# Optimization experiments

Measured on AMD Instinct MI355X. Metric: run time of the kernel, lower is better.

The kernel has to match this reference:

```python
import jax, jax.numpy as jnp
import numpy as np

F_IN = 128
H = 512


def _uniform(key, shape, stdv):
    return jax.random.uniform(key, shape, jnp.float32, -stdv, stdv)


def setup_inputs() -> dict:
    key = jax.random.key(0)
    ks = jax.random.split(key, 20)
    B, T, F = 512, 96, F_IN
    x = jax.random.normal(ks[0], (B, T, F), jnp.float32)
    mask = jax.random.randint(ks[1], (B, T, F), 0, 2).astype(jnp.int32)
    sH = 1.0 / np.sqrt(H)
    sF = 1.0 / np.sqrt(F)
    inp = {
        'x': x,
        'mask': mask,
        # TemporalDecay h: W [H, F], b [H]
        'Wdh': _uniform(ks[2], (H, F), sH), 'bdh': _uniform(ks[3], (H,), sH),
        # TemporalDecay x (diag): W [F, F], b [F]
        'Wdx': _uniform(ks[4], (F, F), sF), 'bdx': _uniform(ks[5], (F,), sF),
        # hist_reg Linear(H, F)
        'Wh': _uniform(ks[6], (F, H), sH), 'bh': _uniform(ks[7], (F,), sH),
        # feat_reg: W [F, F] (off-diagonal mask), b [F]
        'Wf': _uniform(ks[8], (F, F), sF), 'bf': _uniform(ks[9], (F,), sF),
        # weight_combine Linear(2F, F)
        'Wc': _uniform(ks[10], (F, 2 * F), 1.0 / np.sqrt(2 * F)),
        'bc': _uniform(ks[11], (F,), 1.0 / np.sqrt(2 * F)),
        # LSTMCell(2F, H): torch gate order i, f, g, o
        'Wih': _uniform(ks[12], (4 * H, 2 * F), sH),
        'Whh': _uniform(ks[13], (4 * H, H), sH),
        'bih': _uniform(ks[14], (4 * H,), sH),
        'bhh': _uniform(ks[15], (4 * H,), sH),
    }
    return inp


def _rits_forward(x, m, Wdh, bdh, Wdx, bdx, Wh, bh, Wf, bf, Wc, bc, Wih, Whh, bih, bhh):
    B, T, F = x.shape
    eye = jnp.eye(F, dtype=x.dtype)
    Wf_m = Wf * (1.0 - eye)
    Wdx_m = Wdx * eye         # diagonal TemporalDecay

    # compute_delta (freq=1): delta[0]=0; delta[i]=m[i-1]+ (1-m[i-1])*(delta[i-1]+1)
    m_tm = jnp.swapaxes(m, 0, 1)  # [T, B, F]
    def dstep(prev, mp):
        nxt = mp + (1.0 - mp) * (prev + 1.0)
        return nxt, nxt
    _, drest = jax.lax.scan(dstep, jnp.zeros((B, F), x.dtype), m_tm[:-1])
    delta_tm = jnp.concatenate([jnp.zeros((1, B, F), x.dtype), drest], axis=0)

    x_tm = jnp.swapaxes(x, 0, 1)  # [T, B, F]

    def step(carry, inp):
        h, c = carry
        x_s, m_s, d = inp
        gamma_h = jnp.exp(-jax.nn.relu(d @ Wdh.T + bdh))          # [B, H]
        x_h = h @ Wh.T + bh                                        # [B, F]
        x_c = m_s * x_s + (1.0 - m_s) * x_h
        h = h * gamma_h
        z_h = x_c @ Wf_m.T + bf
        gamma_x = jnp.exp(-jax.nn.relu(d @ Wdx_m.T + bdx))
        alpha = jax.nn.sigmoid(jnp.concatenate([gamma_x, m_s], axis=1) @ Wc.T + bc)
        c_h = alpha * z_h + (1.0 - alpha) * x_h
        c_c = m_s * x_s + (1.0 - m_s) * c_h
        inputs = jnp.concatenate([c_c, m_s], axis=1)               # [B, 2F]
        gates = inputs @ Wih.T + bih + h @ Whh.T + bhh             # [B, 4H]
        i_g, f_g, g_g, o_g = jnp.split(gates, 4, axis=1)
        c = jax.nn.sigmoid(f_g) * c + jax.nn.sigmoid(i_g) * jnp.tanh(g_g)
        h = jax.nn.sigmoid(o_g) * jnp.tanh(c)
        return (h, c), (c_c, c_h, z_h, x_h)

    h0 = jnp.zeros((B, H), x.dtype)
    c0 = jnp.zeros((B, H), x.dtype)
    _, (c_c, c_h, z_h, x_h) = jax.lax.scan(step, (h0, c0), (x_tm, m_tm, delta_tm))
    # back to [B, T, F]
    tr = lambda a: jnp.swapaxes(a, 0, 1)
    return tr(c_c), tr(c_h), tr(z_h), tr(x_h)


def reference(x, mask, Wdh, bdh, Wdx, bdx, Wh, bh, Wf, bf, Wc, bc, Wih, Whh, bih, bhh):
    m = mask.astype(x.dtype)
    imputation, c_h, z_h, x_h = _rits_forward(
        x, m, Wdh, bdh, Wdx, bdx, Wh, bh, Wf, bf, Wc, bc, Wih, Whh, bih, bhh)
    return (imputation, (c_h, z_h, x_h))
```

## Files before the change

kernel.cpp:

```cpp
#include <hip/hip_runtime.h>
#include <cstdint>
#include <cstddef>

#define BB 512
#define TT 96
#define FF 128
#define HH 512
#define BTF 6291456
#define BH  262144

typedef unsigned short ushort_t;
typedef __attribute__((ext_vector_type(8))) short bf16x8;
typedef __attribute__((ext_vector_type(4))) float f32x4;

static constexpr size_t OFF_FLAGS = 0;
static constexpr size_t OFF_WDXD  = 2048;
static constexpr size_t OFF_DELTA = 4096;
static constexpr size_t OFF_MBF   = OFF_DELTA + 12582912;
static constexpr size_t OFF_ALPHA = OFF_MBF   + 12582912;
static constexpr size_t OFF_GH    = OFF_ALPHA + 12582912;
static constexpr size_t OFF_H     = OFF_GH    + 50331648;
static constexpr size_t OFF_HDEC  = OFF_H     + 2097152;
static constexpr size_t OFF_CCBF  = OFF_HDEC  + 1048576;

__device__ __forceinline__ float bf2f(ushort_t u) {
  union { unsigned u; float f; } c; c.u = ((unsigned)u) << 16; return c.f;
}
__device__ __forceinline__ ushort_t f2bf(float f) {
  union { float f; unsigned u; } c; c.f = f;
  unsigned x = c.u;
  unsigned r = (x + 0x7FFFu + ((x >> 16) & 1u)) >> 16;
  return (ushort_t)r;
}
__device__ __forceinline__ float lo2f(unsigned p) {
  union { unsigned u; float f; } c; c.u = p << 16; return c.f;
}
__device__ __forceinline__ float hi2f(unsigned p) {
  union { unsigned u; float f; } c; c.u = p & 0xffff0000u; return c.f;
}
__device__ __forceinline__ float sigm(float v) { return 1.0f / (1.0f + __expf(-v)); }

__device__ __forceinline__ bf16x8 cload16(const ushort_t* p) {
  union { unsigned long long q[2]; bf16x8 v; } u;
  unsigned long long* a = (unsigned long long*)p;
  u.q[0] = __hip_atomic_load(a,     __ATOMIC_RELAXED, __HIP_MEMORY_SCOPE_AGENT);
  u.q[1] = __hip_atomic_load(a + 1, __ATOMIC_RELAXED, __HIP_MEMORY_SCOPE_AGENT);
  return u.v;
}
__device__ __forceinline__ float cloadf(const float* p) {
  unsigned v = __hip_atomic_load((const unsigned*)p, __ATOMIC_RELAXED, __HIP_MEMORY_SCOPE_AGENT);
  union { unsigned u; float f; } c; c.u = v; return c.f;
}
__device__ __forceinline__ void cstore8(void* p, unsigned long long v) {
  __hip_atomic_store((unsigned long long*)p, v, __ATOMIC_RELAXED, __HIP_MEMORY_SCOPE_AGENT);
}
__device__ __forceinline__ void cstore4(void* p, unsigned v) {
  __hip_atomic_store((unsigned*)p, v, __ATOMIC_RELAXED, __HIP_MEMORY_SCOPE_AGENT);
}
__device__ __forceinline__ void cstore2(ushort_t* p, ushort_t v) {
  __hip_atomic_store(p, v, __ATOMIC_RELAXED, __HIP_MEMORY_SCOPE_AGENT);
}
__device__ __forceinline__ float rdlane_f(float v, int sl) {
  return __int_as_float(__builtin_amdgcn_readlane(__float_as_int(v), sl));
}

__global__ void k_cvt(const float* __restrict__ Wdx, char* __restrict__ ws) {
  int tid = threadIdx.x;
  unsigned* fl = (unsigned*)(ws + OFF_FLAGS);
  fl[tid] = 0; fl[256 + tid] = 0;
  float* wdxd = (float*)(ws + OFF_WDXD);
  if (tid < FF) wdxd[tid] = Wdx[tid * (FF + 1)];
}

__global__ void k_prep(const int* __restrict__ mask, char* __restrict__ ws) {
  ushort_t* delta = (ushort_t*)(ws + OFF_DELTA);
  ushort_t* mbf   = (ushort_t*)(ws + OFF_MBF);
  int gtid = blockIdx.x * 256 + threadIdx.x;
  int b = gtid >> 7, f = gtid & 127;
  const int* mrow = mask + (size_t)b * (TT * FF) + f;
  float dprev = 0.0f;
  for (int t = 0; t < TT; ++t) {
    float d;
    if (t == 0) d = 0.0f;
    else {
      int mp = mrow[(t - 1) * FF];
      d = mp ? 1.0f : dprev + 1.0f;
    }
    dprev = d;
    delta[((size_t)t * BB + b) * FF + f] = f2bf(d);
    int mc = mrow[t * FF];
    mbf[(size_t)b * (TT * FF) + t * FF + f] = f2bf((float)mc);
  }
}

__global__ __launch_bounds__(256, 4) void k_gh(const float* __restrict__ Wdh,
                                               const float* __restrict__ bdh,
                                               char* __restrict__ ws) {
  __shared__ ushort_t A_lds[64 * 136];
  __shared__ ushort_t B_lds[64 * 136];
  const ushort_t* delta = (const ushort_t*)(ws + OFF_DELTA);
  ushort_t* gh = (ushort_t*)(ws + OFF_GH);
  int tid = threadIdx.x;
  int m0 = blockIdx.x * 64;
  int n0 = blockIdx.y * 64;
  for (int v = tid; v < 1024; v += 256) {
    int row = v >> 4, seg = v & 15;
    *(uint4*)&A_lds[row * 136 + seg * 8] =
        *(const uint4*)(delta + ((size_t)(m0 + row)) * FF + seg * 8);
  }
  for (int v = tid; v < 1024; v += 256) {
    int n = v >> 4, seg = v & 15;
    const float* src = Wdh + (size_t)(n0 + n) * FF + seg * 8;
    ushort_t tmp[8];
#pragma unroll
    for (int j = 0; j < 8; ++j) tmp[j] = f2bf(src[j]);
    *(uint4*)&B_lds[n * 136 + seg * 8] = *(const uint4*)tmp;
  }
  __syncthreads();
  int wave = tid >> 6, lane = tid & 63, quad = lane >> 4, lan = lane & 15;
  int mt = wave;
  f32x4 acc[4];
#pragma unroll
  for (int nt = 0; nt < 4; ++nt) acc[nt] = (f32x4){0.f, 0.f, 0.f, 0.f};
  const ushort_t* ab = &A_lds[(mt * 16 + lan) * 136 + quad * 8];
#pragma unroll
  for (int kk = 0; kk < 4; ++kk) {
    bf16x8 af = *(const bf16x8*)(ab + kk * 32);
#pragma unroll
    for (int nt = 0; nt < 4; ++nt) {
      bf16x8 bfv = *(const bf16x8*)(&B_lds[(nt * 16 + lan) * 136 + kk * 32 + quad * 8]);
      acc[nt] = __builtin_amdgcn_mfma_f32_16x16x32_bf16(af, bfv, acc[nt], 0, 0, 0);
    }
  }
#pragma unroll
  for (int nt = 0; nt < 4; ++nt) {
#pragma unroll
    for (int r = 0; r < 4; ++r) {
      int mg = m0 + mt * 16 + quad * 4 + r;
      int nc = n0 + nt * 16 + lan;
      float v = acc[nt][r] + bdh[nc];
      gh[(size_t)mg * HH + nc] = f2bf(__expf(-fmaxf(v, 0.0f)));
    }
  }
}

__global__ __launch_bounds__(256, 4) void k_al(const float* __restrict__ Wc,
                                               const float* __restrict__ bc,
                                               const float* __restrict__ bdx,
                                               char* __restrict__ ws) {
  __shared__ ushort_t A_lds[64 * 136];
  __shared__ ushort_t B_lds[64 * 136];
  const ushort_t* delta = (const ushort_t*)(ws + OFF_DELTA);
  const ushort_t* mbf   = (const ushort_t*)(ws + OFF_MBF);
  const float* wdxd     = (const float*)(ws + OFF_WDXD);
  ushort_t* alpha = (ushort_t*)(ws + OFF_ALPHA);
  int tid = threadIdx.x;
  int m0 = blockIdx.x * 64;
  int n0 = blockIdx.y * 64;
  int wave = tid >> 6, lane = tid & 63, quad = lane >> 4, lan = lane & 15;
  int mt = wave;
  f32x4 acc[4];
#pragma unroll
  for (int nt = 0; nt < 4; ++nt) acc[nt] = (f32x4){0.f, 0.f, 0.f, 0.f};
  for (int c = 0; c < 2; ++c) {
    __syncthreads();
    if (c == 0) {
      for (int v = tid; v < 1024; v += 256) {
        int row = v >> 4, seg = v & 15;
        int mg = m0 + row;
        ushort_t tmp[8];
#pragma unroll
        for (int j = 0; j < 8; ++j) {
          int k = seg * 8 + j;
          float d = bf2f(delta[(size_t)mg * FF + k]);
          float g = __expf(-fmaxf(fmaf(d, wdxd[k], bdx[k]), 0.0f));
          tmp[j] = f2bf(g);
        }
        *(uint4*)&A_lds[row * 136 + seg * 8] = *(const uint4*)tmp;
      }
    } else {
      for (int v = tid; v < 1024; v += 256) {
        int row = v >> 4, seg = v & 15;
        int mg = m0 + row;
        int t = mg >> 9, b = mg & 511;
        *(uint4*)&A_lds[row * 136 + seg * 8] =
            *(const uint4*)(mbf + ((size_t)b * TT + t) * FF + seg * 8);
      }
    }
    for (int v = tid; v < 1024; v += 256) {
      int n = v >> 4, seg = v & 15;
      const float* src = Wc + (size_t)(n0 + n) * 256 + c * 128 + seg * 8;
      ushort_t tmp[8];
#pragma unroll
      for (int j = 0; j < 8; ++j) tmp[j] = f2bf(src[j]);
      *(uint4*)&B_lds[n * 136 + seg * 8] = *(const uint4*)tmp;
    }
    __syncthreads();
    const ushort_t* ab = &A_lds[(mt * 16 + lan) * 136 + quad * 8];
#pragma unroll
    for (int kk = 0; kk < 4; ++kk) {
      bf16x8 af = *(const bf16x8*)(ab + kk * 32);
#pragma unroll
      for (int nt = 0; nt < 4; ++nt) {
        bf16x8 bfv = *(const bf16x8*)(&B_lds[(nt * 16 + lan) * 136 + kk * 32 + quad * 8]);
        acc[nt] = __builtin_amdgcn_mfma_f32_16x16x32_bf16(af, bfv, acc[nt], 0, 0, 0);
      }
    }
  }
#pragma unroll
  for (int nt = 0; nt < 4; ++nt) {
#pragma unroll
    for (int r = 0; r < 4; ++r) {
      int mg = m0 + mt * 16 + quad * 4 + r;
      int nc = n0 + nt * 16 + lan;
      float v = acc[nt][r] + bc[nc];
      alpha[(size_t)mg * FF + nc] = f2bf(sigm(v));
    }
  }
}

__device__ __forceinline__ void bar_arrive(unsigned* cnt) {
  __syncthreads();
  if (threadIdx.x == 0)
    __hip_atomic_fetch_add(cnt, 1u, __ATOMIC_RELAXED, __HIP_MEMORY_SCOPE_AGENT);
}
__device__ __forceinline__ void bar_wait(unsigned* cnt, unsigned target) {
  if (threadIdx.x == 0) {
    while (__hip_atomic_load(cnt, __ATOMIC_RELAXED, __HIP_MEMORY_SCOPE_AGENT) < target)
      __builtin_amdgcn_s_sleep(1);
  }
  __syncthreads();
}

__global__ __launch_bounds__(512, 2) void k_main(
    const float* __restrict__ x, const int* __restrict__ mask,
    const float* __restrict__ Wh, const float* __restrict__ Wf,
    const float* __restrict__ bh, const float* __restrict__ bfr,
    const float* __restrict__ Wih, const float* __restrict__ Whh,
    const float* __restrict__ bih, const float* __restrict__ bhh,
    float* __restrict__ out, char* __restrict__ ws) {
  extern __shared__ char smem[];
  ushort_t* W_lds    = (ushort_t*)smem;
  float* gates_lds   = (float*)(smem + 99328);
  float* bias_lds    = (float*)(smem + 134144);
  float* xh_part     = (float*)(smem + 134400);
  float* xc_s        = (float*)(smem + 142592);

  unsigned* cnts = (unsigned*)(ws + OFF_FLAGS);
  const ushort_t* alpha = (const ushort_t*)(ws + OFF_ALPHA);
  const ushort_t* gh    = (const ushort_t*)(ws + OFF_GH);
  const ushort_t* mbf   = (const ushort_t*)(ws + OFF_MBF);
  float*    hws  = (float*)(ws + OFF_H);
  ushort_t* hdws = (ushort_t*)(ws + OFF_HDEC);
  ushort_t* ccbf = (ushort_t*)(ws + OFF_CCBF);

  const int tid  = threadIdx.x;
  const int wg   = blockIdx.x;
  const int g    = wg & 7;
  const int mwg  = wg >> 3;
  const int ng   = mwg;
  const int wave = tid >> 6, lane = tid & 63, quad = lane >> 4, lan = lane & 15;
  const int mt = wave & 3, khalf = wave >> 2;
  const int r0 = g * 64 + mwg * 2;
  const int arow = g * 64 + mt * 16 + lan;

  unsigned* cntA = cnts + (g * 2 + 0) * 32;
  unsigned* cntB = cnts + (g * 2 + 1) * 32;

  for (int q = tid; q < 4096; q += 512) {
    int n = q >> 6, kq = (q & 63) * 4;
    int r = (n >> 4) * 512 + ng * 16 + (n & 15);
    float4 v = *(const float4*)(Wih + (size_t)r * 256 + kq);
    ushort_t t4[4] = { f2bf(v.x), f2bf(v.y), f2bf(v.z), f2bf(v.w) };
    *(uint2*)&W_lds[n * 776 + kq] = *(const uint2*)t4;
  }
  for (int q = tid; q < 8192; q += 512) {
    int n = q >> 7, kq = (q & 127) * 4;
    int r = (n >> 4) * 512 + ng * 16 + (n & 15);
    float4 v = *(const float4*)(Whh + (size_t)r * 512 + kq);
    ushort_t t4[4] = { f2bf(v.x), f2bf(v.y), f2bf(v.z), f2bf(v.w) };
    *(uint2*)&W_lds[n * 776 + 256 + kq] = *(const uint2*)t4;
  }
  if (tid < 64) {
    int r = (tid >> 4) * 512 + ng * 16 + (tid & 15);
    bias_lds[tid] = bih[r] + bhh[r];
  }

  unsigned wh_p[64];
  {
    const float* s0 = Wh + (size_t)lane * HH + 64 * wave;
    const float* s1 = Wh + (size_t)(lane + 64) * HH + 64 * wave;
#pragma unroll
    for (int i4 = 0; i4 < 16; ++i4) {
      float4 a = *(const float4*)(s0 + i4 * 4);
      float4 b = *(const float4*)(s1 + i4 * 4);
      wh_p[i4 * 4 + 0] = ((unsigned)f2bf(a.x)) | (((unsigned)f2bf(b.x)) << 16);
      wh_p[i4 * 4 + 1] = ((unsigned)f2bf(a.y)) | (((unsigned)f2bf(b.y)) << 16);
      wh_p[i4 * 4 + 2] = ((unsigned)f2bf(a.z)) | (((unsigned)f2bf(b.z)) << 16);
      wh_p[i4 * 4 + 3] = ((unsigned)f2bf(a.w)) | (((unsigned)f2bf(b.w)) << 16);
    }
  }
  unsigned wf_p[16];
  {
    const float* s0 = Wf + (size_t)lane * FF + 16 * wave;
    const float* s1 = Wf + (size_t)(lane + 64) * FF + 16 * wave;
#pragma unroll
    for (int i4 = 0; i4 < 4; ++i4) {
      float4 a = *(const float4*)(s0 + i4 * 4);
      float4 b = *(const float4*)(s1 + i4 * 4);
      wf_p[i4 * 4 + 0] = ((unsigned)f2bf(a.x)) | (((unsigned)f2bf(b.x)) << 16);
      wf_p[i4 * 4 + 1] = ((unsigned)f2bf(a.y)) | (((unsigned)f2bf(b.y)) << 16);
      wf_p[i4 * 4 + 2] = ((unsigned)f2bf(a.z)) | (((unsigned)f2bf(b.z)) << 16);
      wf_p[i4 * 4 + 3] = ((unsigned)f2bf(a.w)) | (((unsigned)f2bf(b.w)) << 16);
    }
  }
  const int fdot = tid & 127;
  float bh_r = 0.f, bfr_r = 0.f, wfd_r = 0.f;
  if (tid < 256) {
    bh_r  = bh[fdot];
    bfr_r = bfr[fdot];
    wfd_r = bf2f(f2bf(Wf[(size_t)fdot * FF + fdot]));
  }

  const int b_l = tid >> 3, jl0 = 2 * (tid & 7);
  const int bglob = g * 64 + b_l, j0 = ng * 16 + jl0;
  cstore8(&hws[(size_t)bglob * HH + j0], 0ull);
  cstore4(&hdws[(size_t)bglob * HH + j0], 0u);
  float c_r0 = 0.f, c_r1 = 0.f;

  unsigned epA = 0, epB = 1;
  bar_arrive(cntB);

  for (int t = 0; t < TT; ++t) {
    float xv = 0.f, mv = 0.f, al = 0.f;
    if (tid < 256) {
      int bl = tid >> 7;
      int b = r0 + bl;
      size_t gix = (size_t)b * (TT * FF) + (size_t)t * FF + fdot;
      xv = x[gix];
      mv = (float)mask[gix];
      al = bf2f(alpha[((size_t)t * BB + b) * FF + fdot]);
    }
    unsigned gh2 = 0;
    if (t < TT - 1)
      gh2 = *(const unsigned*)&gh[((size_t)(t + 1) * BB + bglob) * HH + j0];
    bf16x8 A0[4], A1[4], A2[4];
    if (khalf == 0) {
      const ushort_t* mrow = mbf + ((size_t)arow * TT + t) * FF + quad * 8;
#pragma unroll
      for (int kk = 0; kk < 4; ++kk) A0[kk] = *(const bf16x8*)(mrow + kk * 32);
    }

    bar_wait(cntB, 32u * epB);

    const float* hbuf = hws + (size_t)(t & 1) * BH;
    float h0r = cloadf(hbuf + (size_t)r0 * HH + 64 * wave + lane);
    float h1r = cloadf(hbuf + (size_t)(r0 + 1) * HH + 64 * wave + lane);
    {
      const ushort_t* hdec = hdws + (size_t)(t & 1) * BH;
      const ushort_t* hrow = hdec + (size_t)arow * HH + quad * 8;
      if (khalf == 0) {
#pragma unroll
        for (int kk = 0; kk < 4; ++kk) A1[kk] = cload16(hrow + kk * 32);
      } else {
#pragma unroll
        for (int kk = 0; kk < 4; ++kk) A0[kk] = cload16(hrow + 128 + kk * 32);
#pragma unroll
        for (int kk = 0; kk < 4; ++kk) A1[kk] = cload16(hrow + 256 + kk * 32);
#pragma unroll
        for (int kk = 0; kk < 4; ++kk) A2[kk] = cload16(hrow + 384 + kk * 32);
      }
    }

    f32x4 acc[4];
#pragma unroll
    for (int nt = 0; nt < 4; ++nt) acc[nt] = (f32x4){0.f, 0.f, 0.f, 0.f};
    {
      const int w0 = khalf ? 384 : 128;
      const int w1 = khalf ? 512 : 256;
#pragma unroll
      for (int kk = 0; kk < 4; ++kk) {
#pragma unroll
        for (int nt = 0; nt < 4; ++nt) {
          bf16x8 bv = *(const bf16x8*)(&W_lds[(nt * 16 + lan) * 776 + w0 + kk * 32 + quad * 8]);
          acc[nt] = __builtin_amdgcn_mfma_f32_16x16x32_bf16(A0[kk], bv, acc[nt], 0, 0, 0);
        }
      }
#pragma unroll
      for (int kk = 0; kk < 4; ++kk) {
#pragma unroll
        for (int nt = 0; nt < 4; ++nt) {
          bf16x8 bv = *(const bf16x8*)(&W_lds[(nt * 16 + lan) * 776 + w1 + kk * 32 + quad * 8]);
          acc[nt] = __builtin_amdgcn_mfma_f32_16x16x32_bf16(A1[kk], bv, acc[nt], 0, 0, 0);
        }
      }
      if (khalf == 1) {
#pragma unroll
        for (int kk = 0; kk < 4; ++kk) {
#pragma unroll
          for (int nt = 0; nt < 4; ++nt) {
            bf16x8 bv = *(const bf16x8*)(&W_lds[(nt * 16 + lan) * 776 + 640 + kk * 32 + quad * 8]);
            acc[nt] = __builtin_amdgcn_mfma_f32_16x16x32_bf16(A2[kk], bv, acc[nt], 0, 0, 0);
          }
        }
#pragma unroll
        for (int nt = 0; nt < 4; ++nt)
#pragma unroll
          for (int r = 0; r < 4; ++r)
            gates_lds[(64 + mt * 16 + quad * 4 + r) * 68 + nt * 16 + lan] = acc[nt][r];
      }
    }

    {
      float a00 = 0.f, a01 = 0.f, a10 = 0.f, a11 = 0.f;
#pragma unroll
      for (int k = 0; k < 64; ++k) {
        float hk0 = rdlane_f(h0r, k);
        float hk1 = rdlane_f(h1r, k);
        unsigned wp = wh_p[k];
        float w0 = lo2f(wp), w1 = hi2f(wp);
        a00 = fmaf(w0, hk0, a00);
        a10 = fmaf(w1, hk0, a10);
        a01 = fmaf(w0, hk1, a01);
        a11 = fmaf(w1, hk1, a11);
      }
      xh_part[(wave * 2 + 0) * 128 + lane]      = a00;
      xh_part[(wave * 2 + 0) * 128 + 64 + lane] = a10;
      xh_part[(wave * 2 + 1) * 128 + lane]      = a01;
      xh_part[(wave * 2 + 1) * 128 + 64 + lane] = a11;
    }
    __syncthreads();

    float xh_r = 0.f;
    if (tid < 256) {
      int bl = tid >> 7;
      float s = bh_r;
#pragma unroll
      for (int w2 = 0; w2 < 8; ++w2) s += xh_part[(w2 * 2 + bl) * 128 + fdot];
      xh_r = s;
      float xcv = fmaf(1.0f - mv, xh_r, mv * xv);
      xc_s[bl * 128 + fdot] = xcv;
    }
    __syncthreads();

    {
      float z00 = 0.f, z01 = 0.f, z10 = 0.f, z11 = 0.f;
      float x0 = xc_s[16 * wave + (lane & 15)];
      float x1 = xc_s[128 + 16 * wave + (lane & 15)];
#pragma unroll
      for (int k = 0; k < 16; ++k) {
        float xk0 = rdlane_f(x0, k);
        float xk1 = rdlane_f(x1, k);
        unsigned wp = wf_p[k];
        float w0 = lo2f(wp), w1 = hi2f(wp);
        z00 = fmaf(w0, xk0, z00);
        z10 = fmaf(w1, xk0, z10);
        z01 = fmaf(w0, xk1, z01);
        z11 = fmaf(w1, xk1, z11);
      }
      xh_part[(wave * 2 + 0) * 128 + lane]      = z00;
      xh_part[(wave * 2 + 0) * 128 + 64 + lane] = z10;
      xh_part[(wave * 2 + 1) * 128 + lane]      = z01;
      xh_part[(wave * 2 + 1) * 128 + 64 + lane] = z11;
    }
    __syncthreads();

    float zh = 0.f, ch = 0.f, cc = 0.f;
    if (tid < 256) {
      int bl = tid >> 7;
      int b = r0 + bl;
      float xcv = xc_s[bl * 128 + fdot];
      float s = bfr_r - xcv * wfd_r;
#pragma unroll
      for (int w2 = 0; w2 < 8; ++w2) s += xh_part[(w2 * 2 + bl) * 128 + fdot];
      zh = s;
      ch = fmaf(al, zh, (1.0f - al) * xh_r);
      cc = fmaf(1.0f - mv, ch, mv * xv);
      cstore2(&ccbf[b * FF + fdot], f2bf(cc));
    }

    bar_arrive(cntA); ++epA;

    if (tid < 256) {
      int bl = tid >> 7;
      int b = r0 + bl;
      size_t ob = (size_t)b * (TT * FF) + (size_t)t * FF + fdot;
      out[ob] = cc;
      out[BTF + ob] = ch;
      out[2 * (size_t)BTF + ob] = zh;
      out[3 * (size_t)BTF + ob] = xh_r;
    }

    bar_wait(cntA, 32u * epA);

    if (khalf == 0) {
      const ushort_t* ccrow = ccbf + (size_t)arow * FF + quad * 8;
      bf16x8 AC[4];
#pragma unroll
      for (int kk = 0; kk < 4; ++kk) AC[kk] = cload16(ccrow + kk * 32);
#pragma unroll
      for (int kk = 0; kk < 4; ++kk) {
#pragma unroll
        for (int nt = 0; nt < 4; ++nt) {
          bf16x8 bv = *(const bf16x8*)(&W_lds[(nt * 16 + lan) * 776 + kk * 32 + quad * 8]);
          acc[nt] = __builtin_amdgcn_mfma_f32_16x16x32_bf16(AC[kk], bv, acc[nt], 0, 0, 0);
        }
      }
#pragma unroll
      for (int nt = 0; nt < 4; ++nt)
#pragma unroll
        for (int r = 0; r < 4; ++r)
          gates_lds[(mt * 16 + quad * 4 + r) * 68 + nt * 16 + lan] = acc[nt][r];
    }
    __syncthreads();

    {
      const float* g0 = &gates_lds[(size_t)b_l * 68 + jl0];
      const float* g1 = &gates_lds[(size_t)(64 + b_l) * 68 + jl0];
      float2 gI = make_float2(g0[0] + g1[0] + bias_lds[jl0],
                              g0[1] + g1[1] + bias_lds[jl0 + 1]);
      float2 gF = make_float2(g0[16] + g1[16] + bias_lds[16 + jl0],
                              g0[17] + g1[17] + bias_lds[16 + jl0 + 1]);
      float2 gG = make_float2(g0[32] + g1[32] + bias_lds[32 + jl0],
                              g0[33] + g1[33] + bias_lds[32 + jl0 + 1]);
      float2 gO = make_float2(g0[48] + g1[48] + bias_lds[48 + jl0],
                              g0[49] + g1[49] + bias_lds[48 + jl0 + 1]);
      c_r0 = fmaf(sigm(gF.x), c_r0, sigm(gI.x) * tanhf(gG.x));
      c_r1 = fmaf(sigm(gF.y), c_r1, sigm(gI.y) * tanhf(gG.y));
      float h0 = sigm(gO.x) * tanhf(c_r0);
      float h1 = sigm(gO.y) * tanhf(c_r1);
      float* hwN = hws + (size_t)((t + 1) & 1) * BH;
      ushort_t* hdN = hdws + (size_t)((t + 1) & 1) * BH;
      union { float2 f; unsigned long long q; } hu; hu.f = make_float2(h0, h1);
      cstore8(&hwN[(size_t)bglob * HH + j0], hu.q);
      float gHa = lo2f(gh2), gHb = hi2f(gh2);
      unsigned hp = ((unsigned)f2bf(h0 * gHa)) | (((unsigned)f2bf(h1 * gHb)) << 16);
      cstore4(&hdN[(size_t)bglob * HH + j0], hp);
    }

    bar_arrive(cntB); ++epB;
  }
}

extern "C" void kernel_launch(void* const* d_in, const int* in_sizes, int n_in,
                              void* d_out, int out_size, void* d_ws, size_t ws_size,
                              hipStream_t stream) {
  (void)in_sizes; (void)n_in; (void)out_size; (void)ws_size;
  const float* x   = (const float*)d_in[0];
  const int*   mask= (const int*)d_in[1];
  const float* Wdh = (const float*)d_in[2];
  const float* bdh = (const float*)d_in[3];
  const float* Wdx = (const float*)d_in[4];
  const float* bdx = (const float*)d_in[5];
  const float* Wh  = (const float*)d_in[6];
  const float* bh  = (const float*)d_in[7];
  const float* Wf  = (const float*)d_in[8];
  const float* bfr = (const float*)d_in[9];
  const float* Wc  = (const float*)d_in[10];
  const float* bc  = (const float*)d_in[11];
  const float* Wih = (const float*)d_in[12];
  const float* Whh = (const float*)d_in[13];
  const float* bih = (const float*)d_in[14];
  const float* bhh = (const float*)d_in[15];
  float* out = (float*)d_out;
  char* ws = (char*)d_ws;

  hipLaunchKernelGGL(k_cvt,  dim3(1),   dim3(256), 0, stream, Wdx, ws);
  hipLaunchKernelGGL(k_prep, dim3(256), dim3(256), 0, stream, mask, ws);
  hipLaunchKernelGGL(k_gh,   dim3(768, 8), dim3(256), 0, stream, Wdh, bdh, ws);
  hipLaunchKernelGGL(k_al,   dim3(768, 2), dim3(256), 0, stream, Wc, bc, bdx, ws);

  hipFuncSetAttribute((const void*)k_main, hipFuncAttributeMaxDynamicSharedMemorySize, 143616);
  void* args[] = { (void*)&x, (void*)&mask, (void*)&Wh, (void*)&Wf, (void*)&bh, (void*)&bfr,
                   (void*)&Wih, (void*)&Whh, (void*)&bih, (void*)&bhh, (void*)&out, (void*)&ws };
  hipLaunchCooperativeKernel((const void*)k_main, dim3(256), dim3(512), args, 143616, stream);
}
```

Measured before the change: 1.586 ms.

## Replace atomic-counter group barrier with per-workgroup epoch flags and pad gates LDS

Each workgroup now publishes its epoch to its own flag slot with a plain atomic store instead of incrementing a shared counter. The waiter uses one wave to poll all 32 flags in parallel and exits when a ballot shows none lag. This removes contention from serialized fetch-add on one cache line across the group. The gates LDS row stride is also padded to 69 floats to reduce bank conflicts, and the flag and LDS layouts are enlarged to match.

```diff
diff --git a/kernel.cpp b/kernel.cpp
--- a/kernel.cpp
+++ b/kernel.cpp
@@ -14,8 +14,8 @@
 typedef __attribute__((ext_vector_type(4))) float f32x4;
 
 static constexpr size_t OFF_FLAGS = 0;
-static constexpr size_t OFF_WDXD  = 2048;
-static constexpr size_t OFF_DELTA = 4096;
+static constexpr size_t OFF_WDXD  = 4096;
+static constexpr size_t OFF_DELTA = 8192;
 static constexpr size_t OFF_MBF   = OFF_DELTA + 12582912;
 static constexpr size_t OFF_ALPHA = OFF_MBF   + 12582912;
 static constexpr size_t OFF_GH    = OFF_ALPHA + 12582912;
@@ -23,6 +23,15 @@
 static constexpr size_t OFF_HDEC  = OFF_H     + 2097152;
 static constexpr size_t OFF_CCBF  = OFF_HDEC  + 1048576;
 
+#define GSTR 69
+
+static constexpr int LDS_W     = 0;
+static constexpr int LDS_GATES = 99328;
+static constexpr int LDS_BIAS  = 134656;
+static constexpr int LDS_XPART = 134912;
+static constexpr int LDS_XC    = 143104;
+static constexpr int LDS_TOTAL = 144128;
+
 __device__ __forceinline__ float bf2f(ushort_t u) {
   union { unsigned u; float f; } c; c.u = ((unsigned)u) << 16; return c.f;
 }
@@ -51,6 +60,9 @@
   unsigned v = __hip_atomic_load((const unsigned*)p, __ATOMIC_RELAXED, __HIP_MEMORY_SCOPE_AGENT);
   union { unsigned u; float f; } c; c.u = v; return c.f;
 }
+__device__ __forceinline__ unsigned cload4u(const unsigned* p) {
+  return __hip_atomic_load(p, __ATOMIC_RELAXED, __HIP_MEMORY_SCOPE_AGENT);
+}
 __device__ __forceinline__ void cstore8(void* p, unsigned long long v) {
   __hip_atomic_store((unsigned long long*)p, v, __ATOMIC_RELAXED, __HIP_MEMORY_SCOPE_AGENT);
 }
@@ -67,7 +79,7 @@
 __global__ void k_cvt(const float* __restrict__ Wdx, char* __restrict__ ws) {
   int tid = threadIdx.x;
   unsigned* fl = (unsigned*)(ws + OFF_FLAGS);
-  fl[tid] = 0; fl[256 + tid] = 0;
+  fl[tid] = 0; fl[256 + tid] = 0; fl[512 + tid] = 0; fl[768 + tid] = 0;
   float* wdxd = (float*)(ws + OFF_WDXD);
   if (tid < FF) wdxd[tid] = Wdx[tid * (FF + 1)];
 }
@@ -219,15 +231,18 @@
   }
 }
 
-__device__ __forceinline__ void bar_arrive(unsigned* cnt) {
+__device__ __forceinline__ void barf_arrive(unsigned* flags, int member, unsigned ep) {
   __syncthreads();
-  if (threadIdx.x == 0)
-    __hip_atomic_fetch_add(cnt, 1u, __ATOMIC_RELAXED, __HIP_MEMORY_SCOPE_AGENT);
-}
-__device__ __forceinline__ void bar_wait(unsigned* cnt, unsigned target) {
-  if (threadIdx.x == 0) {
-    while (__hip_atomic_load(cnt, __ATOMIC_RELAXED, __HIP_MEMORY_SCOPE_AGENT) < target)
+  if (threadIdx.x == 0) cstore4(&flags[member], ep);
+}
+__device__ __forceinline__ void barf_wait(const unsigned* flags, unsigned ep, int lane) {
+  if (threadIdx.x < 64) {
+    const unsigned* p = flags + (lane & 31);
+    while (true) {
+      unsigned v = cload4u(p);
+      if (!__ballot(v < ep)) break;
       __builtin_amdgcn_s_sleep(1);
+    }
   }
   __syncthreads();
 }
@@ -240,13 +255,12 @@
     const float* __restrict__ bih, const float* __restrict__ bhh,
     float* __restrict__ out, char* __restrict__ ws) {
   extern __shared__ char smem[];
-  ushort_t* W_lds    = (ushort_t*)smem;
-  float* gates_lds   = (float*)(smem + 99328);
-  float* bias_lds    = (float*)(smem + 134144);
-  float* xh_part     = (float*)(smem + 134400);
-  float* xc_s        = (float*)(smem + 142592);
-
-  unsigned* cnts = (unsigned*)(ws + OFF_FLAGS);
+  ushort_t* W_lds    = (ushort_t*)(smem + LDS_W);
+  float* gates_lds   = (float*)(smem + LDS_GATES);
+  float* bias_lds    = (float*)(smem + LDS_BIAS);
+  float* xh_part     = (float*)(smem + LDS_XPART);
+  float* xc_s        = (float*)(smem + LDS_XC);
+
   const ushort_t* alpha = (const ushort_t*)(ws + OFF_ALPHA);
   const ushort_t* gh    = (const ushort_t*)(ws + OFF_GH);
   const ushort_t* mbf   = (const ushort_t*)(ws + OFF_MBF);
@@ -264,8 +278,8 @@
   const int r0 = g * 64 + mwg * 2;
   const int arow = g * 64 + mt * 16 + lan;
 
-  unsigned* cntA = cnts + (g * 2 + 0) * 32;
-  unsigned* cntB = cnts + (g * 2 + 1) * 32;
+  unsigned* flagsA = (unsigned*)(ws + OFF_FLAGS) + g * 64;
+  unsigned* flagsB = (unsigned*)(ws + OFF_FLAGS) + (8 + g) * 64;
 
   for (int q = tid; q < 4096; q += 512) {
     int n = q >> 6, kq = (q & 63) * 4;
@@ -329,7 +343,7 @@
   float c_r0 = 0.f, c_r1 = 0.f;
 
   unsigned epA = 0, epB = 1;
-  bar_arrive(cntB);
+  barf_arrive(flagsB, mwg, epB);
 
   for (int t = 0; t < TT; ++t) {
     float xv = 0.f, mv = 0.f, al = 0.f;
@@ -351,7 +365,7 @@
       for (int kk = 0; kk < 4; ++kk) A0[kk] = *(const bf16x8*)(mrow + kk * 32);
     }
 
-    bar_wait(cntB, 32u * epB);
+    barf_wait(flagsB, epB, lane);
 
     const float* hbuf = hws + (size_t)(t & 1) * BH;
     float h0r = cloadf(hbuf + (size_t)r0 * HH + 64 * wave + lane);
@@ -407,7 +421,7 @@
         for (int nt = 0; nt < 4; ++nt)
 #pragma unroll
           for (int r = 0; r < 4; ++r)
-            gates_lds[(64 + mt * 16 + quad * 4 + r) * 68 + nt * 16 + lan] = acc[nt][r];
+            gates_lds[(64 + mt * 16 + quad * 4 + r) * GSTR + nt * 16 + lan] = acc[nt][r];
       }
     }
 
@@ -479,7 +493,8 @@
       cstore2(&ccbf[b * FF + fdot], f2bf(cc));
     }
 
-    bar_arrive(cntA); ++epA;
+    ++epA;
+    barf_arrive(flagsA, mwg, epA);
 
     if (tid < 256) {
       int bl = tid >> 7;
@@ -491,7 +506,7 @@
       out[3 * (size_t)BTF + ob] = xh_r;
     }
 
-    bar_wait(cntA, 32u * epA);
+    barf_wait(flagsA, epA, lane);
 
     if (khalf == 0) {
       const ushort_t* ccrow = ccbf + (size_t)arow * FF + quad * 8;
@@ -510,13 +525,13 @@
       for (int nt = 0; nt < 4; ++nt)
 #pragma unroll
         for (int r = 0; r < 4; ++r)
-          gates_lds[(mt * 16 + quad * 4 + r) * 68 + nt * 16 + lan] = acc[nt][r];
+          gates_lds[(mt * 16 + quad * 4 + r) * GSTR + nt * 16 + lan] = acc[nt][r];
     }
     __syncthreads();
 
     {
-      const float* g0 = &gates_lds[(size_t)b_l * 68 + jl0];
-      const float* g1 = &gates_lds[(size_t)(64 + b_l) * 68 + jl0];
+      const float* g0 = &gates_lds[(size_t)b_l * GSTR + jl0];
+      const float* g1 = &gates_lds[(size_t)(64 + b_l) * GSTR + jl0];
       float2 gI = make_float2(g0[0] + g1[0] + bias_lds[jl0],
                               g0[1] + g1[1] + bias_lds[jl0 + 1]);
       float2 gF = make_float2(g0[16] + g1[16] + bias_lds[16 + jl0],
@@ -538,7 +553,8 @@
       cstore4(&hdN[(size_t)bglob * HH + j0], hp);
     }
 
-    bar_arrive(cntB); ++epB;
+    ++epB;
+    barf_arrive(flagsB, mwg, epB);
   }
 }
 
@@ -570,8 +586,8 @@
   hipLaunchKernelGGL(k_gh,   dim3(768, 8), dim3(256), 0, stream, Wdh, bdh, ws);
   hipLaunchKernelGGL(k_al,   dim3(768, 2), dim3(256), 0, stream, Wc, bc, bdx, ws);
 
-  hipFuncSetAttribute((const void*)k_main, hipFuncAttributeMaxDynamicSharedMemorySize, 143616);
+  hipFuncSetAttribute((const void*)k_main, hipFuncAttributeMaxDynamicSharedMemorySize, LDS_TOTAL);
   void* args[] = { (void*)&x, (void*)&mask, (void*)&Wh, (void*)&Wf, (void*)&bh, (void*)&bfr,
                    (void*)&Wih, (void*)&Whh, (void*)&bih, (void*)&bhh, (void*)&out, (void*)&ws };
-  hipLaunchCooperativeKernel((const void*)k_main, dim3(256), dim3(512), args, 143616, stream);
-}
+  hipLaunchCooperativeKernel((const void*)k_main, dim3(256), dim3(512), args, LDS_TOTAL, stream);
+}
```

Result: slower. 1.659 ms (+4.6%).
